# Performance work log

Hardware: AMD Instinct MI355X
Metric: run time of the kernel (lower is better)

The kernel has to match this reference:

```python
import jax, jax.numpy as jnp
import numpy as np

BETA = 2.0
EPS2 = 0.001 * 0.001
N_CLS = 5  # number of region classes present in mask


def setup_inputs() -> dict:
    key = jax.random.key(0)
    k1, k2, k3 = jax.random.split(key, 3)
    B, C, H, W = 16, 512, 64, 64
    feature_rec = jax.random.normal(k1, (B, C, H, W), dtype=jnp.float32)
    feature_align = jax.random.normal(k2, (B, C, H, W), dtype=jnp.float32)
    mask = jax.random.randint(k3, (B, H, W), 0, N_CLS, dtype=jnp.int32)
    return {"feature_rec": feature_rec, "feature_align": feature_align, "mask": mask}


def reference(feature_rec, feature_align, mask):
    # per-pixel mse averaged over channels -> [B, H, W]
    diff = feature_rec - feature_align
    loss_metric = jnp.mean(diff * diff, axis=1)

    # detached copy used for region reweighting (torch: clone().detach())
    w = jax.lax.stop_gradient(loss_metric)
    B, H, W = w.shape

    # segment-mean per (batch, region-class): replaces the double python loop
    seg = (mask.astype(jnp.int32) + jnp.arange(B, dtype=jnp.int32)[:, None, None] * N_CLS).reshape(-1)
    wf = w.reshape(-1)
    sums = jax.ops.segment_sum(wf, seg, num_segments=B * N_CLS)
    counts = jax.ops.segment_sum(jnp.ones_like(wf), seg, num_segments=B * N_CLS)
    avg = sums / jnp.maximum(counts, 1.0)  # empty regions untouched (never gathered)
    w = avg[seg].reshape(B, H, W)

    wmax = jnp.max(w)
    w = jnp.where(wmax > 0, w / (wmax + EPS2), w + EPS2)
    w = jnp.clip(w, 0.0, 1.0)

    return jnp.mean(loss_metric * (w * BETA + 1.0))
```

## Files before the change

kernel.cpp:

```cpp
#include <hip/hip_runtime.h>

#define Bd 16
#define Cd 512
#define Hd 64
#define Wd 64
#define HWd (Hd * Wd)
#define NCLS 5
#define BETA 2.0f
#define EPS2 (0.001f * 0.001f)

constexpr int CH = 32;
constexpr int NCCHUNK = Cd / CH;
constexpr int PIX_PER_BLOCK = 1024;

__global__ __launch_bounds__(256) void seg_partial_kernel(
    const float* __restrict__ rec, const float* __restrict__ aln,
    const int* __restrict__ mask,
    float* __restrict__ segsum, float* __restrict__ segcnt)
{
    __shared__ float binS[NCLS];
    __shared__ float binC[NCLS];
    const int tid = threadIdx.x;
    if (tid < NCLS) { binS[tid] = 0.0f; binC[tid] = 0.0f; }
    __syncthreads();

    const int b   = blockIdx.y;
    const int hw0 = blockIdx.x * PIX_PER_BLOCK + tid * 4;
    const int c0  = blockIdx.z * CH;

    const size_t base = (size_t)(b * Cd + c0) * HWd + hw0;
    const float4* __restrict__ rv = (const float4*)(rec + base);
    const float4* __restrict__ av = (const float4*)(aln + base);

    float4 acc = make_float4(0.f, 0.f, 0.f, 0.f);
#pragma unroll 8
    for (int c = 0; c < CH; ++c) {
        float4 r = rv[c * (HWd / 4)];
        float4 a = av[c * (HWd / 4)];
        float dx = r.x - a.x, dy = r.y - a.y, dz = r.z - a.z, dw = r.w - a.w;
        acc.x += dx * dx;
        acc.y += dy * dy;
        acc.z += dz * dz;
        acc.w += dw * dw;
    }

    const float scale = 1.0f / (float)Cd;
    const int4 m = *(const int4*)(mask + b * HWd + hw0);
    atomicAdd(&binS[m.x], acc.x * scale);
    atomicAdd(&binS[m.y], acc.y * scale);
    atomicAdd(&binS[m.z], acc.z * scale);
    atomicAdd(&binS[m.w], acc.w * scale);
    if (blockIdx.z == 0) {
        atomicAdd(&binC[m.x], 1.0f);
        atomicAdd(&binC[m.y], 1.0f);
        atomicAdd(&binC[m.z], 1.0f);
        atomicAdd(&binC[m.w], 1.0f);
    }
    __syncthreads();
    if (tid < NCLS) {
        atomicAdd(&segsum[b * NCLS + tid], binS[tid]);
        if (blockIdx.z == 0) atomicAdd(&segcnt[b * NCLS + tid], binC[tid]);
    }
}

__global__ __launch_bounds__(128) void finalize_kernel(
    const float* __restrict__ segsum, const float* __restrict__ segcnt,
    float* __restrict__ out)
{
    __shared__ float sMax[128];
    __shared__ float sSum[128];
    const int t = threadIdx.x;

    float s = 0.0f, cnt = 0.0f;
    if (t < Bd * NCLS) { s = segsum[t]; cnt = segcnt[t]; }
    const float avg = s / fmaxf(cnt, 1.0f);

    sMax[t] = avg;
    __syncthreads();
#pragma unroll
    for (int off = 64; off > 0; off >>= 1) {
        if (t < off) sMax[t] = fmaxf(sMax[t], sMax[t + off]);
        __syncthreads();
    }
    const float wmax = sMax[0];

    float w = (wmax > 0.0f) ? (avg / (wmax + EPS2)) : (avg + EPS2);
    w = fminf(fmaxf(w, 0.0f), 1.0f);

    sSum[t] = s * (w * BETA + 1.0f);
    __syncthreads();
#pragma unroll
    for (int off = 64; off > 0; off >>= 1) {
        if (t < off) sSum[t] += sSum[t + off];
        __syncthreads();
    }
    if (t == 0) out[0] = sSum[0] / (float)(Bd * HWd);
}

extern "C" void kernel_launch(void* const* d_in, const int* in_sizes, int n_in,
                              void* d_out, int out_size, void* d_ws, size_t ws_size,
                              hipStream_t stream) {
    const float* rec  = (const float*)d_in[0];
    const float* aln  = (const float*)d_in[1];
    const int*   mask = (const int*)d_in[2];
    float* out = (float*)d_out;

    float* segsum = (float*)d_ws;
    float* segcnt = segsum + Bd * NCLS;

    hipMemsetAsync(d_ws, 0, 2 * Bd * NCLS * sizeof(float), stream);

    dim3 grid(HWd / PIX_PER_BLOCK, Bd, NCCHUNK);
    seg_partial_kernel<<<grid, 256, 0, stream>>>(rec, aln, mask, segsum, segcnt);
    finalize_kernel<<<1, 128, 0, stream>>>(segsum, segcnt, out);
}
```

Before: 289.0 us.

## Split channels into 4-wide chunks per block and reduce classes via wave shuffles

```diff
diff --git a/kernel.cpp b/kernel.cpp
--- a/kernel.cpp
+++ b/kernel.cpp
@@ -2,64 +2,115 @@
 
 #define Bd 16
 #define Cd 512
-#define Hd 64
-#define Wd 64
-#define HWd (Hd * Wd)
+#define HWd 4096
 #define NCLS 5
 #define BETA 2.0f
 #define EPS2 (0.001f * 0.001f)
 
-constexpr int CH = 32;
-constexpr int NCCHUNK = Cd / CH;
-constexpr int PIX_PER_BLOCK = 1024;
+constexpr int CHB = 4;
+constexpr int NCHUNK = Cd / CHB;
+constexpr int Q4 = HWd / 4;
 
-__global__ __launch_bounds__(256) void seg_partial_kernel(
+__global__ __launch_bounds__(256, 8) void seg_partial_kernel(
     const float* __restrict__ rec, const float* __restrict__ aln,
     const int* __restrict__ mask,
     float* __restrict__ segsum, float* __restrict__ segcnt)
 {
-    __shared__ float binS[NCLS];
-    __shared__ float binC[NCLS];
-    const int tid = threadIdx.x;
-    if (tid < NCLS) { binS[tid] = 0.0f; binC[tid] = 0.0f; }
-    __syncthreads();
+    const int tid   = threadIdx.x;
+    const int b     = blockIdx.y;
+    const int chunk = blockIdx.x;
 
-    const int b   = blockIdx.y;
-    const int hw0 = blockIdx.x * PIX_PER_BLOCK + tid * 4;
-    const int c0  = blockIdx.z * CH;
-
-    const size_t base = (size_t)(b * Cd + c0) * HWd + hw0;
+    const size_t base = ((size_t)b * Cd + (size_t)chunk * CHB) * HWd;
     const float4* __restrict__ rv = (const float4*)(rec + base);
     const float4* __restrict__ av = (const float4*)(aln + base);
+    const int4*   __restrict__ mv = (const int4*)(mask + (size_t)b * HWd);
 
-    float4 acc = make_float4(0.f, 0.f, 0.f, 0.f);
-#pragma unroll 8
-    for (int c = 0; c < CH; ++c) {
-        float4 r = rv[c * (HWd / 4)];
-        float4 a = av[c * (HWd / 4)];
-        float dx = r.x - a.x, dy = r.y - a.y, dz = r.z - a.z, dw = r.w - a.w;
-        acc.x += dx * dx;
-        acc.y += dy * dy;
-        acc.z += dz * dz;
-        acc.w += dw * dw;
+    float4 acc0 = {0,0,0,0}, acc1 = {0,0,0,0}, acc2 = {0,0,0,0}, acc3 = {0,0,0,0};
+
+#pragma unroll
+    for (int c = 0; c < CHB; ++c) {
+        const float4* r4 = rv + c * Q4;
+        const float4* a4 = av + c * Q4;
+        float4 r0 = r4[tid], r1 = r4[tid + 256], r2 = r4[tid + 512], r3 = r4[tid + 768];
+        float4 a0 = a4[tid], a1 = a4[tid + 256], a2 = a4[tid + 512], a3 = a4[tid + 768];
+        float d;
+        d = r0.x - a0.x; acc0.x += d * d;
+        d = r0.y - a0.y; acc0.y += d * d;
+        d = r0.z - a0.z; acc0.z += d * d;
+        d = r0.w - a0.w; acc0.w += d * d;
+        d = r1.x - a1.x; acc1.x += d * d;
+        d = r1.y - a1.y; acc1.y += d * d;
+        d = r1.z - a1.z; acc1.z += d * d;
+        d = r1.w - a1.w; acc1.w += d * d;
+        d = r2.x - a2.x; acc2.x += d * d;
+        d = r2.y - a2.y; acc2.y += d * d;
+        d = r2.z - a2.z; acc2.z += d * d;
+        d = r2.w - a2.w; acc2.w += d * d;
+        d = r3.x - a3.x; acc3.x += d * d;
+        d = r3.y - a3.y; acc3.y += d * d;
+        d = r3.z - a3.z; acc3.z += d * d;
+        d = r3.w - a3.w; acc3.w += d * d;
     }
 
-    const float scale = 1.0f / (float)Cd;
-    const int4 m = *(const int4*)(mask + b * HWd + hw0);
-    atomicAdd(&binS[m.x], acc.x * scale);
-    atomicAdd(&binS[m.y], acc.y * scale);
-    atomicAdd(&binS[m.z], acc.z * scale);
-    atomicAdd(&binS[m.w], acc.w * scale);
-    if (blockIdx.z == 0) {
-        atomicAdd(&binC[m.x], 1.0f);
-        atomicAdd(&binC[m.y], 1.0f);
-        atomicAdd(&binC[m.z], 1.0f);
-        atomicAdd(&binC[m.w], 1.0f);
+    int4 m0 = mv[tid];
+    int4 m1 = mv[tid + 256];
+    int4 m2 = mv[tid + 512];
+    int4 m3 = mv[tid + 768];
+
+    float cls[NCLS] = {0, 0, 0, 0, 0};
+    {
+        float v[16] = {acc0.x, acc0.y, acc0.z, acc0.w,
+                       acc1.x, acc1.y, acc1.z, acc1.w,
+                       acc2.x, acc2.y, acc2.z, acc2.w,
+                       acc3.x, acc3.y, acc3.z, acc3.w};
+        int   mm[16] = {m0.x, m0.y, m0.z, m0.w,
+                        m1.x, m1.y, m1.z, m1.w,
+                        m2.x, m2.y, m2.z, m2.w,
+                        m3.x, m3.y, m3.z, m3.w};
+#pragma unroll
+        for (int e = 0; e < 16; ++e) {
+#pragma unroll
+            for (int k = 0; k < NCLS; ++k)
+                cls[k] += (mm[e] == k) ? v[e] : 0.0f;
+        }
     }
-    __syncthreads();
-    if (tid < NCLS) {
-        atomicAdd(&segsum[b * NCLS + tid], binS[tid]);
-        if (blockIdx.z == 0) atomicAdd(&segcnt[b * NCLS + tid], binC[tid]);
+
+#pragma unroll
+    for (int k = 0; k < NCLS; ++k) {
+#pragma unroll
+        for (int off = 32; off > 0; off >>= 1)
+            cls[k] += __shfl_down(cls[k], off, 64);
+    }
+    if ((tid & 63) == 0) {
+        const float scale = 1.0f / (float)Cd;
+#pragma unroll
+        for (int k = 0; k < NCLS; ++k)
+            atomicAdd(&segsum[b * NCLS + k], cls[k] * scale);
+    }
+
+    if (chunk == 0) {
+        float cnt[NCLS] = {0, 0, 0, 0, 0};
+        int mm[16] = {m0.x, m0.y, m0.z, m0.w,
+                      m1.x, m1.y, m1.z, m1.w,
+                      m2.x, m2.y, m2.z, m2.w,
+                      m3.x, m3.y, m3.z, m3.w};
+#pragma unroll
+        for (int e = 0; e < 16; ++e) {
+#pragma unroll
+            for (int k = 0; k < NCLS; ++k)
+                cnt[k] += (mm[e] == k) ? 1.0f : 0.0f;
+        }
+#pragma unroll
+        for (int k = 0; k < NCLS; ++k) {
+#pragma unroll
+            for (int off = 32; off > 0; off >>= 1)
+                cnt[k] += __shfl_down(cnt[k], off, 64);
+        }
+        if ((tid & 63) == 0) {
+#pragma unroll
+            for (int k = 0; k < NCLS; ++k)
+                atomicAdd(&segcnt[b * NCLS + k], cnt[k]);
+        }
     }
 }
 
@@ -110,7 +161,7 @@
 
     hipMemsetAsync(d_ws, 0, 2 * Bd * NCLS * sizeof(float), stream);
 
-    dim3 grid(HWd / PIX_PER_BLOCK, Bd, NCCHUNK);
+    dim3 grid(NCHUNK, Bd);
     seg_partial_kernel<<<grid, 256, 0, stream>>>(rec, aln, mask, segsum, segcnt);
     finalize_kernel<<<1, 128, 0, stream>>>(segsum, segcnt, out);
 }
```

Measured after the change: 503.5 us. 1.74x slower.
